# Kernel tuning notes

Measured on AMD Instinct MI355X. Metric: run time of the kernel, lower is better.

Reference implementation:

```python
import jax, jax.numpy as jnp
import numpy as np

GROUPS = 32
EPS = 1e-5

def group_norm(x, gamma, beta):
    B, C, H, W = x.shape
    xg = x.reshape(B, GROUPS, C // GROUPS, H, W)
    mean = xg.mean(axis=(2, 3, 4), keepdims=True)
    var = xg.var(axis=(2, 3, 4), keepdims=True)
    xn = ((xg - mean) * jax.lax.rsqrt(var + EPS)).reshape(B, C, H, W)
    return xn * gamma[None, :, None, None] + beta[None, :, None, None]

def conv1x1(x, w, b):
    # x: [B,C,H,W], w: [O,C], b: [O]
    return jnp.einsum('oc,bchw->bohw', w, x) + b[None, :, None, None]

def setup_inputs() -> dict:
    C = 256
    B, H, W = 32, 32, 32
    key = jax.random.key(0)
    ks = jax.random.split(key, 12)
    s = 0.02
    return {
        'x': jax.random.normal(ks[0], (B, C, H, W), jnp.float32),
        'gn_gamma': jnp.ones((C,), jnp.float32),
        'gn_beta': jnp.zeros((C,), jnp.float32),
        'w_qkv': jax.random.normal(ks[1], (3 * C, C), jnp.float32) * s,
        'b_qkv': jnp.zeros((3 * C,), jnp.float32),
        'w_proj': jax.random.normal(ks[2], (C, C), jnp.float32) * s,
        'b_proj': jnp.zeros((C,), jnp.float32),
        'w_se1': jax.random.normal(ks[3], (C // 4, C), jnp.float32) * s,
        'b_se1': jnp.zeros((C // 4,), jnp.float32),
        'w_se2': jax.random.normal(ks[4], (C, C // 4), jnp.float32) * s,
        'b_se2': jnp.zeros((C,), jnp.float32),
    }

def reference(x, gn_gamma, gn_beta, w_qkv, b_qkv, w_proj, b_proj, w_se1, b_se1, w_se2, b_se2):
    B, C, H, W = x.shape
    N = H * W
    residual = x
    xn = group_norm(x, gn_gamma, gn_beta)
    qkv = conv1x1(xn, w_qkv, b_qkv)            # [B,3C,H,W]
    q, k, v = jnp.split(qkv.reshape(B, 3 * C, N), 3, axis=1)  # each [B,C,N]
    scale = 1.0 / jnp.sqrt(jnp.float32(C))
    scores = jnp.einsum('bcn,bcm->bnm', q, k) * scale          # [B,N,N]
    attn = jax.nn.softmax(scores, axis=-1)
    # torch.bmm(v, attn^T): out[b,c,i] = sum_j v[b,c,j] * attn[b,i,j]
    x_attn = jnp.einsum('bcj,bij->bci', v, attn).reshape(B, C, H, W)
    x_attn = conv1x1(x_attn, w_proj, b_proj)
    # SE channel attention on the ORIGINAL x
    pooled = x.mean(axis=(2, 3))                               # [B,C]
    h1 = jax.nn.relu(pooled @ w_se1.T + b_se1)                 # [B,C//4]
    gate = jax.nn.sigmoid(h1 @ w_se2.T + b_se2)                # [B,C]
    return residual + x_attn * gate[:, :, None, None]
```

## Files before the change

### kernel.cpp

```cpp
#include <hip/hip_runtime.h>

typedef unsigned short u16;
typedef unsigned int u32;
typedef unsigned long long u64;
typedef __attribute__((ext_vector_type(4))) float vfloat4;
typedef __attribute__((ext_vector_type(8))) short vshort8;
typedef __attribute__((ext_vector_type(4))) short vshort4;

#define DEV __device__ __forceinline__

DEV u16 f2b(float f){
  u32 u = __builtin_bit_cast(u32, f);
  u = (u + 0x7fffu + ((u >> 16) & 1u)) >> 16;
  return (u16)u;
}

typedef __attribute__((address_space(3))) u32 as3u;
typedef __attribute__((address_space(1))) u32 as1u;
DEV void gll16(const u16* g, const u16* l){
  __builtin_amdgcn_global_load_lds((const as1u*)(u64)(uintptr_t)g,
                                   (as3u*)(u32)(u64)(uintptr_t)l, 16, 0, 0);
}

__global__ void k_stats(const float* __restrict__ x, float* __restrict__ osum, float* __restrict__ osq){
  int row = blockIdx.x;
  const vfloat4* xr = (const vfloat4*)(x + (size_t)row * 1024);
  vfloat4 v = xr[threadIdx.x];
  float s = v[0]+v[1]+v[2]+v[3];
  float q = v[0]*v[0]+v[1]*v[1]+v[2]*v[2]+v[3]*v[3];
  #pragma unroll
  for (int m = 1; m < 64; m <<= 1){ s += __shfl_xor(s, m); q += __shfl_xor(q, m); }
  __shared__ float ls[4], lq[4];
  int w = threadIdx.x >> 6;
  if ((threadIdx.x & 63) == 0){ ls[w] = s; lq[w] = q; }
  __syncthreads();
  if (threadIdx.x == 0){
    osum[row] = ls[0]+ls[1]+ls[2]+ls[3];
    osq[row]  = lq[0]+lq[1]+lq[2]+lq[3];
  }
}

__global__ void k_prep(const float* __restrict__ sum, const float* __restrict__ sq,
                       const float* __restrict__ gamma, const float* __restrict__ beta,
                       const float* __restrict__ w_se1, const float* __restrict__ b_se1,
                       const float* __restrict__ w_se2, const float* __restrict__ b_se2,
                       float* __restrict__ a_scale, float* __restrict__ bsh, float* __restrict__ gate){
  int b = blockIdx.x, c = threadIdx.x;
  __shared__ float ssh[256], qsh[256], pooled[256], h1[64], meang[32], rstdg[32];
  float s = sum[b*256 + c], q = sq[b*256 + c];
  ssh[c] = s; qsh[c] = q; pooled[c] = s * (1.f/1024.f);
  __syncthreads();
  if (c < 32){
    float gs = 0.f, gq = 0.f;
    #pragma unroll
    for (int i = 0; i < 8; i++){ gs += ssh[c*8+i]; gq += qsh[c*8+i]; }
    float mean = gs * (1.f/8192.f);
    float var  = gq * (1.f/8192.f) - mean*mean;
    meang[c] = mean; rstdg[c] = rsqrtf(var + 1e-5f);
  }
  __syncthreads();
  float rs = rstdg[c>>3], mn = meang[c>>3], g = gamma[c];
  a_scale[b*256+c] = rs*g;
  bsh[b*256+c]     = beta[c] - mn*rs*g;
  if (c < 64){
    float acc = b_se1[c];
    const float* wr = w_se1 + c*256;
    for (int i = 0; i < 256; i++) acc += pooled[i]*wr[i];
    h1[c] = fmaxf(acc, 0.f);
  }
  __syncthreads();
  float acc = b_se2[c];
  const float* wr2 = w_se2 + c*64;
  #pragma unroll
  for (int j = 0; j < 64; j++) acc += h1[j]*wr2[j];
  gate[b*256+c] = 1.f / (1.f + __expf(-acc));
}

__global__ void k_wcvt(const float* __restrict__ wq, const float* __restrict__ wp,
                       u16* __restrict__ wqb, u16* __restrict__ wpb){
  int i = blockIdx.x*256 + threadIdx.x;
  if (i < 196608) wqb[i] = f2b(wq[i]);
  else            wpb[i-196608] = f2b(wp[i-196608]);
}

__global__ void k_xt(const float* __restrict__ x, const float* __restrict__ a_s,
                     const float* __restrict__ bsh, u16* __restrict__ xs_t){
  __shared__ float t[64][65];
  int b = blockIdx.z, c0 = blockIdx.y*64, n0 = blockIdx.x*64;
  int tid = threadIdx.x;
  int rr = tid >> 4, cc = (tid & 15)*4;
  #pragma unroll
  for (int itr = 0; itr < 4; itr++){
    int r = rr + itr*16;
    int c = c0 + r;
    float a = a_s[b*256 + c], bs = bsh[b*256 + c];
    vfloat4 v = *(const vfloat4*)(x + ((size_t)(b*256 + c))*1024 + n0 + cc);
    t[r][cc]   = v[0]*a + bs;
    t[r][cc+1] = v[1]*a + bs;
    t[r][cc+2] = v[2]*a + bs;
    t[r][cc+3] = v[3]*a + bs;
  }
  __syncthreads();
  int cl = tid & 63, rg = tid >> 6;
  #pragma unroll
  for (int it2 = 0; it2 < 16; it2++){
    int nl = rg*16 + it2;
    xs_t[((size_t)b*1024 + n0 + nl)*256 + c0 + cl] = f2b(t[cl][nl]);
  }
}

__global__ __launch_bounds__(256) void k_qkv(
    const u16* __restrict__ wq_b, const u16* __restrict__ xs_t,
    const float* __restrict__ b_qkv,
    u16* __restrict__ qt, u16* __restrict__ kph, u16* __restrict__ vph){
  __shared__ u16 Alds[128*40];
  __shared__ u16 Blds[128*40];
  int b  = blockIdx.z;
  int o0 = blockIdx.y * 128;
  int n0 = blockIdx.x * 128;
  int tid = threadIdx.x;
  int w = tid >> 6, lane = tid & 63, lo = lane & 15, hi = lane >> 4;
  int wr = w >> 1, wc = w & 1;
  vfloat4 acc[4][4];
  #pragma unroll
  for (int i = 0; i < 4; i++)
    #pragma unroll
    for (int j = 0; j < 4; j++) acc[i][j] = vfloat4{0.f,0.f,0.f,0.f};

  for (int ks = 0; ks < 8; ks++){
    int c0 = ks*32;
    __syncthreads();
    #pragma unroll
    for (int i = 0; i < 2; i++){
      int cid = tid + i*256;
      int row = cid >> 2, h4 = cid & 3;
      vshort8 a = *(const vshort8*)(wq_b + (o0+row)*256 + c0 + h4*8);
      *(vshort8*)(Alds + row*40 + h4*8) = a;
      vshort8 bl = *(const vshort8*)(xs_t + ((size_t)b*1024 + n0 + row)*256 + c0 + h4*8);
      *(vshort8*)(Blds + row*40 + h4*8) = bl;
    }
    __syncthreads();
    vshort8 af[4], bf[4];
    #pragma unroll
    for (int of = 0; of < 4; of++) af[of] = *(const vshort8*)(Alds + (wr*64+of*16+lo)*40 + hi*8);
    #pragma unroll
    for (int nf = 0; nf < 4; nf++) bf[nf] = *(const vshort8*)(Blds + (wc*64+nf*16+lo)*40 + hi*8);
    #pragma unroll
    for (int of = 0; of < 4; of++)
      #pragma unroll
      for (int nf = 0; nf < 4; nf++)
        acc[of][nf] = __builtin_amdgcn_mfma_f32_16x16x32_bf16(af[of], bf[nf], acc[of][nf], 0, 0, 0);
  }

  int kind = blockIdx.y >> 1;
  #pragma unroll
  for (int of = 0; of < 4; of++){
    int ob = o0 + wr*64 + of*16 + hi*4;
    vfloat4 bq = *(const vfloat4*)(b_qkv + ob);
    #pragma unroll
    for (int nf = 0; nf < 4; nf++){
      int n = n0 + wc*64 + nf*16 + lo;
      int tile = n >> 5, j = n & 31;
      vfloat4 val = acc[of][nf];
      #pragma unroll
      for (int r = 0; r < 4; r++) val[r] += bq[r];
      if (kind == 0){
        vshort4 p;
        #pragma unroll
        for (int r = 0; r < 4; r++) p[r] = (short)f2b(val[r] * 0.09016844f);
        *(vshort4*)(qt + ((size_t)b*1024 + n)*256 + ob) = p;
      } else if (kind == 1){
        vshort4 p;
        #pragma unroll
        for (int r = 0; r < 4; r++) p[r] = (short)f2b(val[r]);
        int cx = (ob - 256) ^ ((j & 7) << 3);
        *(vshort4*)(kph + ((size_t)b << 18) + tile*8192 + j*256 + cx) = p;
      } else {
        int pos = ((j >> 2) & 3)*8 + ((j >> 4) << 2) + (j & 3);
        #pragma unroll
        for (int r = 0; r < 4; r++){
          int c = ob - 512 + r;
          int off = ((c >> 1) << 6) + (((((c & 1) << 5) + pos)) ^ (((c >> 1) & 7) << 3));
          vph[((size_t)b << 18) + tile*8192 + off] = f2b(val[r]);
        }
      }
    }
  }
}

__global__ __launch_bounds__(256, 1) void k_attn(
    const u16* __restrict__ qt, const u16* __restrict__ kph, const u16* __restrict__ vph,
    const u16* __restrict__ wp_b, const float* __restrict__ b_proj,
    const float* __restrict__ gate, const float* __restrict__ x,
    float* __restrict__ out){
  __shared__ u16 smem[33792];
  int b = blockIdx.y, i0 = blockIdx.x * 128;
  int tid = threadIdx.x, w = tid >> 6, lane = tid & 63, lo = lane & 15, hi = lane >> 4;

  vshort8 qf[2][8];
  #pragma unroll
  for (int f = 0; f < 2; f++){
    int iq = i0 + w*32 + f*16 + lo;
    #pragma unroll
    for (int ct = 0; ct < 8; ct++)
      qf[f][ct] = *(const vshort8*)(qt + ((size_t)b*1024 + iq)*256 + ct*32 + hi*8);
  }

  vfloat4 Oacc[16][2];
  #pragma unroll
  for (int i = 0; i < 16; i++){ Oacc[i][0] = vfloat4{0.f,0.f,0.f,0.f}; Oacc[i][1] = vfloat4{0.f,0.f,0.f,0.f}; }
  float m_run[2] = {-1e30f, -1e30f}, l_run[2] = {0.f, 0.f};

  int kswz = (lo & 7) << 3;
  int koff[8];
  #pragma unroll
  for (int ct = 0; ct < 8; ct++) koff[ct] = (ct*32 + hi*8) ^ kswz;
  int vbase = (lo >> 1)*64 + ((((lo & 1) << 5) + hi*8) ^ (((lo >> 1) & 7) << 3));

  const u16* kbat = kph + ((size_t)b << 18);
  const u16* vbat = vph + ((size_t)b << 18);

  auto STAGE = [&](int tt, int buf){
    const u16* ks = kbat + (size_t)tt * 8192;
    const u16* vs = vbat + (size_t)tt * 8192;
    u16* kd = smem + buf * 8192;
    u16* vd = smem + 16384 + buf * 8192;
    #pragma unroll
    for (int s = 0; s < 4; s++){
      int ch = (s*256 + tid) * 8;
      gll16(ks + ch, kd + ch);
      gll16(vs + ch, vd + ch);
    }
  };

  STAGE(0, 0);
  __syncthreads();

  for (int t = 0; t < 32; t++){
    int buf = t & 1;
    if (t < 31) STAGE(t + 1, buf ^ 1);
    const u16* Kb = smem + buf*8192;
    const u16* Vb = smem + 16384 + buf*8192;

    vfloat4 st[2][2];
    st[0][0] = vfloat4{0.f,0.f,0.f,0.f}; st[0][1] = vfloat4{0.f,0.f,0.f,0.f};
    st[1][0] = vfloat4{0.f,0.f,0.f,0.f}; st[1][1] = vfloat4{0.f,0.f,0.f,0.f};
    #pragma unroll
    for (int ct = 0; ct < 8; ct++){
      vshort8 k0 = *(const vshort8*)(Kb + lo*256 + koff[ct]);
      vshort8 k1 = *(const vshort8*)(Kb + (16 + lo)*256 + koff[ct]);
      st[0][0] = __builtin_amdgcn_mfma_f32_16x16x32_bf16(k0, qf[0][ct], st[0][0], 0,0,0);
      st[0][1] = __builtin_amdgcn_mfma_f32_16x16x32_bf16(k0, qf[1][ct], st[0][1], 0,0,0);
      st[1][0] = __builtin_amdgcn_mfma_f32_16x16x32_bf16(k1, qf[0][ct], st[1][0], 0,0,0);
      st[1][1] = __builtin_amdgcn_mfma_f32_16x16x32_bf16(k1, qf[1][ct], st[1][1], 0,0,0);
    }

    float pm[2];
    #pragma unroll
    for (int f = 0; f < 2; f++){
      float a = fmaxf(fmaxf(st[0][f][0], st[0][f][1]), fmaxf(st[0][f][2], st[0][f][3]));
      float c = fmaxf(fmaxf(st[1][f][0], st[1][f][1]), fmaxf(st[1][f][2], st[1][f][3]));
      float p = fmaxf(a, c);
      p = fmaxf(p, __shfl_xor(p, 16));
      p = fmaxf(p, __shfl_xor(p, 32));
      pm[f] = p;
    }
    bool ok = (pm[0] - m_run[0] <= 8.f) && (pm[1] - m_run[1] <= 8.f);
    if (!__all(ok)){
      #pragma unroll
      for (int f = 0; f < 2; f++){
        float mn = fmaxf(m_run[f], pm[f]);
        float corr = exp2f(m_run[f] - mn);
        #pragma unroll
        for (int i = 0; i < 16; i++) Oacc[i][f] *= corr;
        l_run[f] *= corr;
        m_run[f] = mn;
      }
    }
    vshort8 pf[2];
    #pragma unroll
    for (int f = 0; f < 2; f++){
      float p[8], ps = 0.f;
      #pragma unroll
      for (int e = 0; e < 4; e++){
        p[e]   = exp2f(st[0][f][e] - m_run[f]);
        p[4+e] = exp2f(st[1][f][e] - m_run[f]);
        ps += p[e] + p[4+e];
      }
      ps += __shfl_xor(ps, 16); ps += __shfl_xor(ps, 32);
      l_run[f] += ps;
      #pragma unroll
      for (int e2 = 0; e2 < 8; e2++) pf[f][e2] = (short)f2b(p[e2]);
    }

    #pragma unroll
    for (int ct2 = 0; ct2 < 16; ct2++){
      vshort8 vf = *(const vshort8*)(Vb + ct2*512 + vbase);
      Oacc[ct2][0] = __builtin_amdgcn_mfma_f32_16x16x32_bf16(vf, pf[0], Oacc[ct2][0], 0,0,0);
      Oacc[ct2][1] = __builtin_amdgcn_mfma_f32_16x16x32_bf16(vf, pf[1], Oacc[ct2][1], 0,0,0);
    }
    __syncthreads();
  }

  float inv[2] = {1.f / l_run[0], 1.f / l_run[1]};
  u16* Ol = smem;
  #pragma unroll
  for (int f = 0; f < 2; f++)
    #pragma unroll
    for (int ct2 = 0; ct2 < 16; ct2++){
      vshort4 p;
      #pragma unroll
      for (int r = 0; r < 4; r++) p[r] = (short)f2b(Oacc[ct2][f][r] * inv[f]);
      *(vshort4*)(Ol + (w*32 + f*16 + lo)*264 + ct2*16 + hi*4) = p;
    }
  __syncthreads();

  vfloat4 acc2[4][8];
  #pragma unroll
  for (int i = 0; i < 4; i++)
    #pragma unroll
    for (int j = 0; j < 8; j++) acc2[i][j] = vfloat4{0.f,0.f,0.f,0.f};
  #pragma unroll
  for (int ct = 0; ct < 8; ct++){
    vshort8 wf[4], ofr[8];
    #pragma unroll
    for (int o4 = 0; o4 < 4; o4++)
      wf[o4] = *(const vshort8*)(wp_b + (w*64 + o4*16 + lo)*256 + ct*32 + hi*8);
    #pragma unroll
    for (int i4 = 0; i4 < 8; i4++)
      ofr[i4] = *(const vshort8*)(Ol + (i4*16 + lo)*264 + ct*32 + hi*8);
    #pragma unroll
    for (int o4 = 0; o4 < 4; o4++)
      #pragma unroll
      for (int i4 = 0; i4 < 8; i4++)
        acc2[o4][i4] = __builtin_amdgcn_mfma_f32_16x16x32_bf16(wf[o4], ofr[i4], acc2[o4][i4], 0,0,0);
  }

  #pragma unroll
  for (int o4 = 0; o4 < 4; o4++){
    int ob = w*64 + o4*16 + hi*4;
    vfloat4 bp = *(const vfloat4*)(b_proj + ob);
    vfloat4 gt = *(const vfloat4*)(gate + b*256 + ob);
    #pragma unroll
    for (int i4 = 0; i4 < 8; i4++){
      int n = i0 + i4*16 + lo;
      #pragma unroll
      for (int r = 0; r < 4; r++){
        size_t idx = ((size_t)(b*256) + ob + r)*1024 + n;
        out[idx] = x[idx] + (acc2[o4][i4][r] + bp[r]) * gt[r];
      }
    }
  }
}

extern "C" void kernel_launch(void* const* d_in, const int* in_sizes, int n_in,
                              void* d_out, int out_size, void* d_ws, size_t ws_size,
                              hipStream_t stream){
  const float* x      = (const float*)d_in[0];
  const float* gamma  = (const float*)d_in[1];
  const float* beta   = (const float*)d_in[2];
  const float* w_qkv  = (const float*)d_in[3];
  const float* b_qkv  = (const float*)d_in[4];
  const float* w_proj = (const float*)d_in[5];
  const float* b_proj = (const float*)d_in[6];
  const float* w_se1  = (const float*)d_in[7];
  const float* b_se1  = (const float*)d_in[8];
  const float* w_se2  = (const float*)d_in[9];
  const float* b_se2  = (const float*)d_in[10];
  float* out = (float*)d_out;
  char* ws = (char*)d_ws;

  float* sum  = (float*)(ws + 0);
  float* sq   = (float*)(ws + 32768);
  float* a_s  = (float*)(ws + 65536);
  float* bsh  = (float*)(ws + 98304);
  float* gate = (float*)(ws + 131072);
  u16* wq_b   = (u16*)(ws + 163840);
  u16* wp_b   = (u16*)(ws + 557056);
  u16* xs_t   = (u16*)(ws + 688128);
  u16* qt     = (u16*)(ws + 17465344);
  u16* kph    = (u16*)(ws + 34242560);
  u16* vph    = (u16*)(ws + 51019776);

  k_stats<<<8192, 256, 0, stream>>>(x, sum, sq);
  k_wcvt <<<1024, 256, 0, stream>>>(w_qkv, w_proj, wq_b, wp_b);
  k_prep <<<32,   256, 0, stream>>>(sum, sq, gamma, beta, w_se1, b_se1, w_se2, b_se2, a_s, bsh, gate);
  k_xt   <<<dim3(16,4,32), 256, 0, stream>>>(x, a_s, bsh, xs_t);
  k_qkv  <<<dim3(8,6,32),  256, 0, stream>>>(wq_b, xs_t, b_qkv, qt, kph, vph);
  k_attn <<<dim3(8,32),    256, 0, stream>>>(qt, kph, vph, wp_b, b_proj, gate, x, out);
}
```

Before: 130.8 us.

## Split attention keys across wave pairs, load V directly from global, XCD-aware block mapping

The attention kernel now processes 64 query rows per block, with two wave groups each handling alternating key tiles (split-K). The partial softmax states and outputs are merged through shared memory at the end. V is stored in plain channel-major layout and read straight from global memory into registers instead of being staged in LDS, which halves the LDS footprint so two blocks can be resident per CU. Both the QKV and attention grids are flattened and remapped so each XCD handles whole batches for L2 locality, and s_setprio is added around the MFMA loops. The extra merge pass and the uncoalesced-style global V loads add cost and latency risk.

New measurement: 244.8 us. 1.87x slower.

```diff
diff --git a/kernel.cpp b/kernel.cpp
--- a/kernel.cpp
+++ b/kernel.cpp
@@ -112,12 +112,15 @@
 __global__ __launch_bounds__(256) void k_qkv(
     const u16* __restrict__ wq_b, const u16* __restrict__ xs_t,
     const float* __restrict__ b_qkv,
-    u16* __restrict__ qt, u16* __restrict__ kph, u16* __restrict__ vph){
+    u16* __restrict__ qt, u16* __restrict__ kph, u16* __restrict__ vv){
   __shared__ u16 Alds[128*40];
   __shared__ u16 Blds[128*40];
-  int b  = blockIdx.z;
-  int o0 = blockIdx.y * 128;
-  int n0 = blockIdx.x * 128;
+  int bid = blockIdx.x;
+  int xcd = bid & 7, idx = bid >> 3;
+  int b   = xcd*4 + idx/48;
+  int rem = idx % 48;
+  int o0 = (rem >> 3) * 128;
+  int n0 = (rem & 7) * 128;
   int tid = threadIdx.x;
   int w = tid >> 6, lane = tid & 63, lo = lane & 15, hi = lane >> 4;
   int wr = w >> 1, wc = w & 1;
@@ -152,7 +155,7 @@
         acc[of][nf] = __builtin_amdgcn_mfma_f32_16x16x32_bf16(af[of], bf[nf], acc[of][nf], 0, 0, 0);
   }
 
-  int kind = blockIdx.y >> 1;
+  int kind = o0 >> 8;
   #pragma unroll
   for (int of = 0; of < 4; of++){
     int ob = o0 + wr*64 + of*16 + hi*4;
@@ -176,31 +179,32 @@
         int cx = (ob - 256) ^ ((j & 7) << 3);
         *(vshort4*)(kph + ((size_t)b << 18) + tile*8192 + j*256 + cx) = p;
       } else {
-        int pos = ((j >> 2) & 3)*8 + ((j >> 4) << 2) + (j & 3);
         #pragma unroll
-        for (int r = 0; r < 4; r++){
-          int c = ob - 512 + r;
-          int off = ((c >> 1) << 6) + (((((c & 1) << 5) + pos)) ^ (((c >> 1) & 7) << 3));
-          vph[((size_t)b << 18) + tile*8192 + off] = f2b(val[r]);
-        }
+        for (int r = 0; r < 4; r++)
+          vv[((size_t)b*256 + (ob - 512 + r))*1024 + n] = f2b(val[r]);
       }
     }
   }
 }
 
-__global__ __launch_bounds__(256, 1) void k_attn(
-    const u16* __restrict__ qt, const u16* __restrict__ kph, const u16* __restrict__ vph,
+__global__ __launch_bounds__(256, 2) void k_attn(
+    const u16* __restrict__ qt, const u16* __restrict__ kph, const u16* __restrict__ vv,
     const u16* __restrict__ wp_b, const float* __restrict__ b_proj,
     const float* __restrict__ gate, const float* __restrict__ x,
     float* __restrict__ out){
-  __shared__ u16 smem[33792];
-  int b = blockIdx.y, i0 = blockIdx.x * 128;
+  __shared__ u16 smem[32768];
+  __shared__ float Ml[4][2][16], Ll[4][2][16];
+  int bid = blockIdx.x;
+  int xcd = bid & 7, idx = bid >> 3;
+  int b = xcd*4 + (idx >> 4);
+  int i0 = (idx & 15) * 64;
   int tid = threadIdx.x, w = tid >> 6, lane = tid & 63, lo = lane & 15, hi = lane >> 4;
+  int g = w >> 1, r = w & 1;
 
   vshort8 qf[2][8];
   #pragma unroll
   for (int f = 0; f < 2; f++){
-    int iq = i0 + w*32 + f*16 + lo;
+    int iq = i0 + r*32 + f*16 + lo;
     #pragma unroll
     for (int ct = 0; ct < 8; ct++)
       qf[f][ct] = *(const vshort8*)(qt + ((size_t)b*1024 + iq)*256 + ct*32 + hi*8);
@@ -215,36 +219,34 @@
   int koff[8];
   #pragma unroll
   for (int ct = 0; ct < 8; ct++) koff[ct] = (ct*32 + hi*8) ^ kswz;
-  int vbase = (lo >> 1)*64 + ((((lo & 1) << 5) + hi*8) ^ (((lo >> 1) & 7) << 3));
 
   const u16* kbat = kph + ((size_t)b << 18);
-  const u16* vbat = vph + ((size_t)b << 18);
-
-  auto STAGE = [&](int tt, int buf){
-    const u16* ks = kbat + (size_t)tt * 8192;
-    const u16* vs = vbat + (size_t)tt * 8192;
-    u16* kd = smem + buf * 8192;
-    u16* vd = smem + 16384 + buf * 8192;
-    #pragma unroll
-    for (int s = 0; s < 4; s++){
-      int ch = (s*256 + tid) * 8;
-      gll16(ks + ch, kd + ch);
-      gll16(vs + ch, vd + ch);
+  const u16* vvb  = vv  + ((size_t)b << 18);
+
+  auto STAGE = [&](int tile, int buf){
+    const u16* src = kbat + (size_t)tile * 8192;
+    u16* dst = smem + g*16384 + buf*8192;
+    int tg = tid & 127;
+    #pragma unroll
+    for (int s = 0; s < 8; s++){
+      int ch = (s*128 + tg)*8;
+      gll16(src + ch, dst + ch);
     }
   };
 
-  STAGE(0, 0);
-  __syncthreads();
-
-  for (int t = 0; t < 32; t++){
-    int buf = t & 1;
-    if (t < 31) STAGE(t + 1, buf ^ 1);
-    const u16* Kb = smem + buf*8192;
-    const u16* Vb = smem + 16384 + buf*8192;
+  STAGE(g, 0);
+  __syncthreads();
+
+  for (int rd = 0; rd < 16; rd++){
+    int buf = rd & 1;
+    int jt = (2*rd + g)*32;
+    if (rd < 15) STAGE(2*(rd+1) + g, buf ^ 1);
+    const u16* Kb = smem + g*16384 + buf*8192;
 
     vfloat4 st[2][2];
     st[0][0] = vfloat4{0.f,0.f,0.f,0.f}; st[0][1] = vfloat4{0.f,0.f,0.f,0.f};
     st[1][0] = vfloat4{0.f,0.f,0.f,0.f}; st[1][1] = vfloat4{0.f,0.f,0.f,0.f};
+    __builtin_amdgcn_s_setprio(1);
     #pragma unroll
     for (int ct = 0; ct < 8; ct++){
       vshort8 k0 = *(const vshort8*)(Kb + lo*256 + koff[ct]);
@@ -254,6 +256,15 @@
       st[1][0] = __builtin_amdgcn_mfma_f32_16x16x32_bf16(k1, qf[0][ct], st[1][0], 0,0,0);
       st[1][1] = __builtin_amdgcn_mfma_f32_16x16x32_bf16(k1, qf[1][ct], st[1][1], 0,0,0);
     }
+    __builtin_amdgcn_s_setprio(0);
+
+    vshort4 va0[8], va1[8];
+    #pragma unroll
+    for (int c8 = 0; c8 < 8; c8++){
+      const u16* vp = vvb + ((size_t)(c8*16 + lo))*1024 + jt + hi*4;
+      va0[c8] = *(const vshort4*)vp;
+      va1[c8] = *(const vshort4*)(vp + 16);
+    }
 
     float pm[2];
     #pragma unroll
@@ -265,8 +276,8 @@
       p = fmaxf(p, __shfl_xor(p, 32));
       pm[f] = p;
     }
-    bool ok = (pm[0] - m_run[0] <= 8.f) && (pm[1] - m_run[1] <= 8.f);
-    if (!__all(ok)){
+    bool okd = (pm[0] - m_run[0] <= 8.f) && (pm[1] - m_run[1] <= 8.f);
+    if (!__all(okd)){
       #pragma unroll
       for (int f = 0; f < 2; f++){
         float mn = fmaxf(m_run[f], pm[f]);
@@ -293,46 +304,95 @@
       for (int e2 = 0; e2 < 8; e2++) pf[f][e2] = (short)f2b(p[e2]);
     }
 
-    #pragma unroll
-    for (int ct2 = 0; ct2 < 16; ct2++){
-      vshort8 vf = *(const vshort8*)(Vb + ct2*512 + vbase);
-      Oacc[ct2][0] = __builtin_amdgcn_mfma_f32_16x16x32_bf16(vf, pf[0], Oacc[ct2][0], 0,0,0);
-      Oacc[ct2][1] = __builtin_amdgcn_mfma_f32_16x16x32_bf16(vf, pf[1], Oacc[ct2][1], 0,0,0);
-    }
+    __builtin_amdgcn_s_setprio(1);
+    #pragma unroll
+    for (int c8 = 0; c8 < 8; c8++){
+      const u16* vp = vvb + ((size_t)((c8+8)*16 + lo))*1024 + jt + hi*4;
+      vshort4 nb0 = *(const vshort4*)vp;
+      vshort4 nb1 = *(const vshort4*)(vp + 16);
+      vshort8 vf = __builtin_shufflevector(va0[c8], va1[c8], 0,1,2,3,4,5,6,7);
+      Oacc[c8][0] = __builtin_amdgcn_mfma_f32_16x16x32_bf16(vf, pf[0], Oacc[c8][0], 0,0,0);
+      Oacc[c8][1] = __builtin_amdgcn_mfma_f32_16x16x32_bf16(vf, pf[1], Oacc[c8][1], 0,0,0);
+      va0[c8] = nb0; va1[c8] = nb1;
+    }
+    #pragma unroll
+    for (int c8 = 0; c8 < 8; c8++){
+      vshort8 vf = __builtin_shufflevector(va0[c8], va1[c8], 0,1,2,3,4,5,6,7);
+      Oacc[c8+8][0] = __builtin_amdgcn_mfma_f32_16x16x32_bf16(vf, pf[0], Oacc[c8+8][0], 0,0,0);
+      Oacc[c8+8][1] = __builtin_amdgcn_mfma_f32_16x16x32_bf16(vf, pf[1], Oacc[c8+8][1], 0,0,0);
+    }
+    __builtin_amdgcn_s_setprio(0);
     __syncthreads();
   }
 
-  float inv[2] = {1.f / l_run[0], 1.f / l_run[1]};
+  if (hi == 0){ Ml[w][0][lo] = m_run[0]; Ml[w][1][lo] = m_run[1]; }
+  __syncthreads();
+  int pw = w ^ 2;
+  #pragma unroll
+  for (int f = 0; f < 2; f++){
+    float mp = Ml[pw][f][lo];
+    float mm = fmaxf(m_run[f], mp);
+    float sc = exp2f(m_run[f] - mm);
+    l_run[f] *= sc;
+    #pragma unroll
+    for (int i = 0; i < 16; i++) Oacc[i][f] *= sc;
+  }
+  if (hi == 0){ Ll[w][0][lo] = l_run[0]; Ll[w][1][lo] = l_run[1]; }
+  float* freg = (float*)smem;
+  if (g == 1){
+    #pragma unroll
+    for (int f = 0; f < 2; f++)
+      #pragma unroll
+      for (int i = 0; i < 16; i++)
+        *(vfloat4*)(freg + f*8192 + r*4096 + i*256 + lane*4) = Oacc[i][f];
+  }
+  __syncthreads();
+
   u16* Ol = smem;
-  #pragma unroll
-  for (int f = 0; f < 2; f++)
-    #pragma unroll
-    for (int ct2 = 0; ct2 < 16; ct2++){
-      vshort4 p;
-      #pragma unroll
-      for (int r = 0; r < 4; r++) p[r] = (short)f2b(Oacc[ct2][f][r] * inv[f]);
-      *(vshort4*)(Ol + (w*32 + f*16 + lo)*264 + ct2*16 + hi*4) = p;
-    }
-  __syncthreads();
-
-  vfloat4 acc2[4][8];
+  if (g == 0){
+    float inv[2];
+    #pragma unroll
+    for (int f = 0; f < 2; f++){
+      float lsum = l_run[f] + Ll[pw][f][lo];
+      inv[f] = 1.f / lsum;
+      #pragma unroll
+      for (int i = 0; i < 16; i++)
+        Oacc[i][f] += *(const vfloat4*)(freg + f*8192 + r*4096 + i*256 + lane*4);
+    }
+    #pragma unroll
+    for (int f = 0; f < 2; f++)
+      #pragma unroll
+      for (int i = 0; i < 16; i++){
+        vshort4 p;
+        #pragma unroll
+        for (int e = 0; e < 4; e++) p[e] = (short)f2b(Oacc[i][f][e] * inv[f]);
+        int irow = r*32 + f*16 + lo;
+        int coff = (i*16 + hi*4) ^ ((irow & 7) << 3);
+        *(vshort4*)(Ol + irow*256 + coff) = p;
+      }
+  }
+  __syncthreads();
+
+  vfloat4 acc2[4][4];
   #pragma unroll
   for (int i = 0; i < 4; i++)
     #pragma unroll
-    for (int j = 0; j < 8; j++) acc2[i][j] = vfloat4{0.f,0.f,0.f,0.f};
+    for (int j = 0; j < 4; j++) acc2[i][j] = vfloat4{0.f,0.f,0.f,0.f};
   #pragma unroll
   for (int ct = 0; ct < 8; ct++){
-    vshort8 wf[4], ofr[8];
+    vshort8 wf[4], ofr[4];
     #pragma unroll
     for (int o4 = 0; o4 < 4; o4++)
       wf[o4] = *(const vshort8*)(wp_b + (w*64 + o4*16 + lo)*256 + ct*32 + hi*8);
     #pragma unroll
-    for (int i4 = 0; i4 < 8; i4++)
-      ofr[i4] = *(const vshort8*)(Ol + (i4*16 + lo)*264 + ct*32 + hi*8);
+    for (int i4 = 0; i4 < 4; i4++){
+      int irow = i4*16 + lo;
+      ofr[i4] = *(const vshort8*)(Ol + irow*256 + ((ct*32 + hi*8) ^ ((irow & 7) << 3)));
+    }
     #pragma unroll
     for (int o4 = 0; o4 < 4; o4++)
       #pragma unroll
-      for (int i4 = 0; i4 < 8; i4++)
+      for (int i4 = 0; i4 < 4; i4++)
         acc2[o4][i4] = __builtin_amdgcn_mfma_f32_16x16x32_bf16(wf[o4], ofr[i4], acc2[o4][i4], 0,0,0);
   }
 
@@ -342,12 +402,12 @@
     vfloat4 bp = *(const vfloat4*)(b_proj + ob);
     vfloat4 gt = *(const vfloat4*)(gate + b*256 + ob);
     #pragma unroll
-    for (int i4 = 0; i4 < 8; i4++){
+    for (int i4 = 0; i4 < 4; i4++){
       int n = i0 + i4*16 + lo;
       #pragma unroll
-      for (int r = 0; r < 4; r++){
-        size_t idx = ((size_t)(b*256) + ob + r)*1024 + n;
-        out[idx] = x[idx] + (acc2[o4][i4][r] + bp[r]) * gt[r];
+      for (int e = 0; e < 4; e++){
+        size_t idxo = ((size_t)(b*256) + ob + e)*1024 + n;
+        out[idxo] = x[idxo] + (acc2[o4][i4][e] + bp[e]) * gt[e];
       }
     }
   }
@@ -380,12 +440,12 @@
   u16* xs_t   = (u16*)(ws + 688128);
   u16* qt     = (u16*)(ws + 17465344);
   u16* kph    = (u16*)(ws + 34242560);
-  u16* vph    = (u16*)(ws + 51019776);
+  u16* vv     = (u16*)(ws + 51019776);
 
   k_stats<<<8192, 256, 0, stream>>>(x, sum, sq);
   k_wcvt <<<1024, 256, 0, stream>>>(w_qkv, w_proj, wq_b, wp_b);
   k_prep <<<32,   256, 0, stream>>>(sum, sq, gamma, beta, w_se1, b_se1, w_se2, b_se2, a_s, bsh, gate);
   k_xt   <<<dim3(16,4,32), 256, 0, stream>>>(x, a_s, bsh, xs_t);
-  k_qkv  <<<dim3(8,6,32),  256, 0, stream>>>(wq_b, xs_t, b_qkv, qt, kph, vph);
-  k_attn <<<dim3(8,32),    256, 0, stream>>>(qt, kph, vph, wp_b, b_proj, gate, x, out);
-}
+  k_qkv  <<<1536, 256, 0, stream>>>(wq_b, xs_t, b_qkv, qt, kph, vv);
+  k_attn <<<512,  256, 0, stream>>>(qt, kph, vv, wp_b, b_proj, gate, x, out);
+}
```

## Triple-buffer K/V staging in attention and remap blocks to XCDs by batch

Applied to the files above, without the earlier changes.

The attention kernel moves from a double-buffered to a triple-buffered LDS pipeline. It issues the prefetch two tiles ahead after the QK MFMAs, and replaces the full __syncthreads with a partial vmcnt wait plus s_barrier. MFMA sections are wrapped in s_setprio. Both the QKV and attention kernels now use a flat 1D grid whose block indices map each batch onto a single XCD, aiming to improve L2 locality for shared K/V and weights. This raises LDS use to 96KB and depends on vmcnt counting being correct for the outstanding async loads.

Result: slower. 140.2 us (+7.2%).

```diff
diff --git a/kernel.cpp b/kernel.cpp
--- a/kernel.cpp
+++ b/kernel.cpp
@@ -115,9 +115,12 @@
     u16* __restrict__ qt, u16* __restrict__ kph, u16* __restrict__ vph){
   __shared__ u16 Alds[128*40];
   __shared__ u16 Blds[128*40];
-  int b  = blockIdx.z;
-  int o0 = blockIdx.y * 128;
-  int n0 = blockIdx.x * 128;
+  int bid = blockIdx.x;
+  int xcd = bid & 7, idx = bid >> 3;
+  int b   = xcd*4 + idx/48;
+  int rem = idx % 48;
+  int o0 = (rem >> 3) * 128;
+  int n0 = (rem & 7) * 128;
   int tid = threadIdx.x;
   int w = tid >> 6, lane = tid & 63, lo = lane & 15, hi = lane >> 4;
   int wr = w >> 1, wc = w & 1;
@@ -152,7 +155,7 @@
         acc[of][nf] = __builtin_amdgcn_mfma_f32_16x16x32_bf16(af[of], bf[nf], acc[of][nf], 0, 0, 0);
   }
 
-  int kind = blockIdx.y >> 1;
+  int kind = o0 >> 8;
   #pragma unroll
   for (int of = 0; of < 4; of++){
     int ob = o0 + wr*64 + of*16 + hi*4;
@@ -193,8 +196,11 @@
     const u16* __restrict__ wp_b, const float* __restrict__ b_proj,
     const float* __restrict__ gate, const float* __restrict__ x,
     float* __restrict__ out){
-  __shared__ u16 smem[33792];
-  int b = blockIdx.y, i0 = blockIdx.x * 128;
+  __shared__ u16 smem[49152];
+  int bid = blockIdx.x;
+  int xcd = bid & 7, idx = bid >> 3;
+  int b = xcd*4 + (idx >> 3);
+  int i0 = (idx & 7) * 128;
   int tid = threadIdx.x, w = tid >> 6, lane = tid & 63, lo = lane & 15, hi = lane >> 4;
 
   vshort8 qf[2][8];
@@ -220,11 +226,11 @@
   const u16* kbat = kph + ((size_t)b << 18);
   const u16* vbat = vph + ((size_t)b << 18);
 
-  auto STAGE = [&](int tt, int buf){
+  auto STAGE = [&](int tt, int slot){
     const u16* ks = kbat + (size_t)tt * 8192;
     const u16* vs = vbat + (size_t)tt * 8192;
-    u16* kd = smem + buf * 8192;
-    u16* vd = smem + 16384 + buf * 8192;
+    u16* kd = smem + slot * 8192;
+    u16* vd = smem + 24576 + slot * 8192;
     #pragma unroll
     for (int s = 0; s < 4; s++){
       int ch = (s*256 + tid) * 8;
@@ -234,17 +240,21 @@
   };
 
   STAGE(0, 0);
-  __syncthreads();
-
+  STAGE(1, 1);
+  asm volatile("s_waitcnt vmcnt(8)" ::: "memory");
+  __builtin_amdgcn_sched_barrier(0);
+  __builtin_amdgcn_s_barrier();
+  __builtin_amdgcn_sched_barrier(0);
+
+  int slot = 0;
   for (int t = 0; t < 32; t++){
-    int buf = t & 1;
-    if (t < 31) STAGE(t + 1, buf ^ 1);
-    const u16* Kb = smem + buf*8192;
-    const u16* Vb = smem + 16384 + buf*8192;
+    const u16* Kb = smem + slot*8192;
+    const u16* Vb = smem + 24576 + slot*8192;
 
     vfloat4 st[2][2];
     st[0][0] = vfloat4{0.f,0.f,0.f,0.f}; st[0][1] = vfloat4{0.f,0.f,0.f,0.f};
     st[1][0] = vfloat4{0.f,0.f,0.f,0.f}; st[1][1] = vfloat4{0.f,0.f,0.f,0.f};
+    __builtin_amdgcn_s_setprio(1);
     #pragma unroll
     for (int ct = 0; ct < 8; ct++){
       vshort8 k0 = *(const vshort8*)(Kb + lo*256 + koff[ct]);
@@ -254,6 +264,12 @@
       st[1][0] = __builtin_amdgcn_mfma_f32_16x16x32_bf16(k1, qf[0][ct], st[1][0], 0,0,0);
       st[1][1] = __builtin_amdgcn_mfma_f32_16x16x32_bf16(k1, qf[1][ct], st[1][1], 0,0,0);
     }
+    __builtin_amdgcn_s_setprio(0);
+
+    if (t < 30){
+      int s2 = slot + 2; if (s2 >= 3) s2 -= 3;
+      STAGE(t + 2, s2);
+    }
 
     float pm[2];
     #pragma unroll
@@ -265,8 +281,8 @@
       p = fmaxf(p, __shfl_xor(p, 32));
       pm[f] = p;
     }
-    bool ok = (pm[0] - m_run[0] <= 8.f) && (pm[1] - m_run[1] <= 8.f);
-    if (!__all(ok)){
+    bool okd = (pm[0] - m_run[0] <= 8.f) && (pm[1] - m_run[1] <= 8.f);
+    if (!__all(okd)){
       #pragma unroll
       for (int f = 0; f < 2; f++){
         float mn = fmaxf(m_run[f], pm[f]);
@@ -293,16 +309,30 @@
       for (int e2 = 0; e2 < 8; e2++) pf[f][e2] = (short)f2b(p[e2]);
     }
 
+    __builtin_amdgcn_s_setprio(1);
     #pragma unroll
     for (int ct2 = 0; ct2 < 16; ct2++){
       vshort8 vf = *(const vshort8*)(Vb + ct2*512 + vbase);
       Oacc[ct2][0] = __builtin_amdgcn_mfma_f32_16x16x32_bf16(vf, pf[0], Oacc[ct2][0], 0,0,0);
       Oacc[ct2][1] = __builtin_amdgcn_mfma_f32_16x16x32_bf16(vf, pf[1], Oacc[ct2][1], 0,0,0);
     }
-    __syncthreads();
+    __builtin_amdgcn_s_setprio(0);
+
+    if (t < 30){
+      asm volatile("s_waitcnt vmcnt(8)" ::: "memory");
+    } else {
+      asm volatile("s_waitcnt vmcnt(0)" ::: "memory");
+    }
+    __builtin_amdgcn_sched_barrier(0);
+    __builtin_amdgcn_s_barrier();
+    __builtin_amdgcn_sched_barrier(0);
+
+    slot++; if (slot == 3) slot = 0;
   }
 
   float inv[2] = {1.f / l_run[0], 1.f / l_run[1]};
+  asm volatile("s_waitcnt vmcnt(0)" ::: "memory");
+  __syncthreads();
   u16* Ol = smem;
   #pragma unroll
   for (int f = 0; f < 2; f++)
@@ -345,9 +375,9 @@
     for (int i4 = 0; i4 < 8; i4++){
       int n = i0 + i4*16 + lo;
       #pragma unroll
-      for (int r = 0; r < 4; r++){
-        size_t idx = ((size_t)(b*256) + ob + r)*1024 + n;
-        out[idx] = x[idx] + (acc2[o4][i4][r] + bp[r]) * gt[r];
+      for (int e = 0; e < 4; e++){
+        size_t idxo = ((size_t)(b*256) + ob + e)*1024 + n;
+        out[idxo] = x[idxo] + (acc2[o4][i4][e] + bp[e]) * gt[e];
       }
     }
   }
@@ -386,6 +416,6 @@
   k_wcvt <<<1024, 256, 0, stream>>>(w_qkv, w_proj, wq_b, wp_b);
   k_prep <<<32,   256, 0, stream>>>(sum, sq, gamma, beta, w_se1, b_se1, w_se2, b_se2, a_s, bsh, gate);
   k_xt   <<<dim3(16,4,32), 256, 0, stream>>>(x, a_s, bsh, xs_t);
-  k_qkv  <<<dim3(8,6,32),  256, 0, stream>>>(wq_b, xs_t, b_qkv, qt, kph, vph);
-  k_attn <<<dim3(8,32),    256, 0, stream>>>(qt, kph, vph, wp_b, b_proj, gate, x, out);
-}
+  k_qkv  <<<1536, 256, 0, stream>>>(wq_b, xs_t, b_qkv, qt, kph, vph);
+  k_attn <<<256,  256, 0, stream>>>(qt, kph, vph, wp_b, b_proj, gate, x, out);
+}
```

## Switch attention to 32x32x16 MFMA with new K/V swizzles and XCD-aware block mapping

Applied to the files above, without the earlier changes.

Rewrites the flash-attention inner loop to use 32x32x16 bf16 MFMA tiles instead of 16x16x32, with one query row per lane pair. The K and V layouts written by the QKV kernel are re-swizzled to match the new fragment access pattern. Both the QKV and attention grids become 1D with an XCD-aware remap so that blocks of the same batch share an XCD's L2. It also adds s_setprio around the MFMA sections and packs P with v_cvt_pk_bf16_f32. The aim is fewer MFMA and LDS instructions and less shuffle reduction per tile, at the cost of larger accumulator register pressure and the risk of subtle layout mismatches.

New measurement: 120.0 us (median of 3 runs). 1.09x faster.

```diff
diff --git a/kernel.cpp b/kernel.cpp
--- a/kernel.cpp
+++ b/kernel.cpp
@@ -4,8 +4,10 @@
 typedef unsigned int u32;
 typedef unsigned long long u64;
 typedef __attribute__((ext_vector_type(4))) float vfloat4;
+typedef __attribute__((ext_vector_type(16))) float vfloat16;
 typedef __attribute__((ext_vector_type(8))) short vshort8;
 typedef __attribute__((ext_vector_type(4))) short vshort4;
+typedef __attribute__((ext_vector_type(4))) u32 vuint4;
 
 #define DEV __device__ __forceinline__
 
@@ -115,9 +117,12 @@
     u16* __restrict__ qt, u16* __restrict__ kph, u16* __restrict__ vph){
   __shared__ u16 Alds[128*40];
   __shared__ u16 Blds[128*40];
-  int b  = blockIdx.z;
-  int o0 = blockIdx.y * 128;
-  int n0 = blockIdx.x * 128;
+  int bid = blockIdx.x;
+  int xcd = bid & 7, idx = bid >> 3;
+  int b   = xcd*4 + idx/48;
+  int rem = idx % 48;
+  int o0 = (rem >> 3) * 128;
+  int n0 = (rem & 7) * 128;
   int tid = threadIdx.x;
   int w = tid >> 6, lane = tid & 63, lo = lane & 15, hi = lane >> 4;
   int wr = w >> 1, wc = w & 1;
@@ -152,7 +157,7 @@
         acc[of][nf] = __builtin_amdgcn_mfma_f32_16x16x32_bf16(af[of], bf[nf], acc[of][nf], 0, 0, 0);
   }
 
-  int kind = blockIdx.y >> 1;
+  int kind = o0 >> 8;
   #pragma unroll
   for (int of = 0; of < 4; of++){
     int ob = o0 + wr*64 + of*16 + hi*4;
@@ -173,14 +178,17 @@
         vshort4 p;
         #pragma unroll
         for (int r = 0; r < 4; r++) p[r] = (short)f2b(val[r]);
-        int cx = (ob - 256) ^ ((j & 7) << 3);
-        *(vshort4*)(kph + ((size_t)b << 18) + tile*8192 + j*256 + cx) = p;
+        int cx = ob - 256;
+        int slot = (cx >> 3) ^ j;
+        *(vshort4*)(kph + ((size_t)b << 18) + tile*8192 + j*256 + slot*8 + (cx & 7)) = p;
       } else {
-        int pos = ((j >> 2) & 3)*8 + ((j >> 4) << 2) + (j & 3);
+        int m2 = (j >> 4) & 1, q2 = (j >> 2) & 1;
+        int e2 = (j & 3) | ((j & 8) >> 1);
         #pragma unroll
         for (int r = 0; r < 4; r++){
           int c = ob - 512 + r;
-          int off = ((c >> 1) << 6) + (((((c & 1) << 5) + pos)) ^ (((c >> 1) & 7) << 3));
+          int a2 = c >> 2;
+          int off = a2*128 + (c & 3)*32 + ((((m2 << 1) | q2) ^ (a2 & 3)) << 3) + e2;
           vph[((size_t)b << 18) + tile*8192 + off] = f2b(val[r]);
         }
       }
@@ -194,28 +202,34 @@
     const float* __restrict__ gate, const float* __restrict__ x,
     float* __restrict__ out){
   __shared__ u16 smem[33792];
-  int b = blockIdx.y, i0 = blockIdx.x * 128;
+  int bid = blockIdx.x;
+  int xcd = bid & 7, idx = bid >> 3;
+  int b = xcd*4 + (idx >> 3);
+  int i0 = (idx & 7) * 128;
   int tid = threadIdx.x, w = tid >> 6, lane = tid & 63, lo = lane & 15, hi = lane >> 4;
-
-  vshort8 qf[2][8];
-  #pragma unroll
-  for (int f = 0; f < 2; f++){
-    int iq = i0 + w*32 + f*16 + lo;
-    #pragma unroll
-    for (int ct = 0; ct < 8; ct++)
-      qf[f][ct] = *(const vshort8*)(qt + ((size_t)b*1024 + iq)*256 + ct*32 + hi*8);
-  }
-
-  vfloat4 Oacc[16][2];
-  #pragma unroll
-  for (int i = 0; i < 16; i++){ Oacc[i][0] = vfloat4{0.f,0.f,0.f,0.f}; Oacc[i][1] = vfloat4{0.f,0.f,0.f,0.f}; }
-  float m_run[2] = {-1e30f, -1e30f}, l_run[2] = {0.f, 0.f};
-
-  int kswz = (lo & 7) << 3;
-  int koff[8];
-  #pragma unroll
-  for (int ct = 0; ct < 8; ct++) koff[ct] = (ct*32 + hi*8) ^ kswz;
-  int vbase = (lo >> 1)*64 + ((((lo & 1) << 5) + hi*8) ^ (((lo >> 1) & 7) << 3));
+  int jj = lane & 31, q = lane >> 5;
+
+  int iq = i0 + w*32 + jj;
+  vshort8 qf[16];
+  #pragma unroll
+  for (int kk = 0; kk < 16; kk++)
+    qf[kk] = *(const vshort8*)(qt + ((size_t)b*1024 + iq)*256 + kk*16 + q*8);
+
+  vfloat16 Oacc[8];
+  #pragma unroll
+  for (int ct = 0; ct < 8; ct++)
+    #pragma unroll
+    for (int e = 0; e < 16; e++) Oacc[ct][e] = 0.f;
+  float m_run = -1e30f, l_run = 0.f;
+
+  int koff[16];
+  #pragma unroll
+  for (int kk = 0; kk < 16; kk++)
+    koff[kk] = jj*256 + ((((kk << 1) | q) ^ jj) << 3);
+  int a0 = jj >> 2;
+  int vb = a0*128 + (jj & 3)*32;
+  int xm0 = ((q)       ^ (a0 & 3)) << 3;
+  int xm1 = ((2 | q)   ^ (a0 & 3)) << 3;
 
   const u16* kbat = kph + ((size_t)b << 18);
   const u16* vbat = vph + ((size_t)b << 18);
@@ -242,76 +256,73 @@
     const u16* Kb = smem + buf*8192;
     const u16* Vb = smem + 16384 + buf*8192;
 
-    vfloat4 st[2][2];
-    st[0][0] = vfloat4{0.f,0.f,0.f,0.f}; st[0][1] = vfloat4{0.f,0.f,0.f,0.f};
-    st[1][0] = vfloat4{0.f,0.f,0.f,0.f}; st[1][1] = vfloat4{0.f,0.f,0.f,0.f};
+    vfloat16 stA, stB;
+    #pragma unroll
+    for (int e = 0; e < 16; e++){ stA[e] = 0.f; stB[e] = 0.f; }
+    __builtin_amdgcn_s_setprio(1);
+    #pragma unroll
+    for (int kk = 0; kk < 16; kk += 2){
+      vshort8 k0 = *(const vshort8*)(Kb + koff[kk]);
+      vshort8 k1 = *(const vshort8*)(Kb + koff[kk+1]);
+      stA = __builtin_amdgcn_mfma_f32_32x32x16_bf16(k0, qf[kk],   stA, 0,0,0);
+      stB = __builtin_amdgcn_mfma_f32_32x32x16_bf16(k1, qf[kk+1], stB, 0,0,0);
+    }
+    __builtin_amdgcn_s_setprio(0);
+    vfloat16 st = stA + stB;
+
+    float pml = st[0];
+    #pragma unroll
+    for (int e = 1; e < 16; e++) pml = fmaxf(pml, st[e]);
+    if (!__all(pml - m_run <= 8.f)){
+      float po = fmaxf(pml, __shfl_xor(pml, 32));
+      float mn = fmaxf(m_run, po);
+      float corr = exp2f(m_run - mn);
+      #pragma unroll
+      for (int ct = 0; ct < 8; ct++) Oacc[ct] *= corr;
+      l_run *= corr;
+      m_run = mn;
+    }
+
+    float pv[16]; float ls = 0.f;
+    #pragma unroll
+    for (int e = 0; e < 16; e++){ pv[e] = exp2f(st[e] - m_run); ls += pv[e]; }
+    l_run += ls;
+
+    u32 pw[8];
+    #pragma unroll
+    for (int rr = 0; rr < 4; rr++){
+      asm("v_cvt_pk_bf16_f32 %0, %1, %2" : "=v"(pw[rr])   : "v"(pv[2*rr]),   "v"(pv[2*rr+1]));
+      asm("v_cvt_pk_bf16_f32 %0, %1, %2" : "=v"(pw[4+rr]) : "v"(pv[8+2*rr]), "v"(pv[8+2*rr+1]));
+    }
+    vshort8 pf0 = __builtin_bit_cast(vshort8, vuint4{pw[0], pw[1], pw[2], pw[3]});
+    vshort8 pf1 = __builtin_bit_cast(vshort8, vuint4{pw[4], pw[5], pw[6], pw[7]});
+
+    __builtin_amdgcn_s_setprio(1);
     #pragma unroll
     for (int ct = 0; ct < 8; ct++){
-      vshort8 k0 = *(const vshort8*)(Kb + lo*256 + koff[ct]);
-      vshort8 k1 = *(const vshort8*)(Kb + (16 + lo)*256 + koff[ct]);
-      st[0][0] = __builtin_amdgcn_mfma_f32_16x16x32_bf16(k0, qf[0][ct], st[0][0], 0,0,0);
-      st[0][1] = __builtin_amdgcn_mfma_f32_16x16x32_bf16(k0, qf[1][ct], st[0][1], 0,0,0);
-      st[1][0] = __builtin_amdgcn_mfma_f32_16x16x32_bf16(k1, qf[0][ct], st[1][0], 0,0,0);
-      st[1][1] = __builtin_amdgcn_mfma_f32_16x16x32_bf16(k1, qf[1][ct], st[1][1], 0,0,0);
-    }
-
-    float pm[2];
-    #pragma unroll
-    for (int f = 0; f < 2; f++){
-      float a = fmaxf(fmaxf(st[0][f][0], st[0][f][1]), fmaxf(st[0][f][2], st[0][f][3]));
-      float c = fmaxf(fmaxf(st[1][f][0], st[1][f][1]), fmaxf(st[1][f][2], st[1][f][3]));
-      float p = fmaxf(a, c);
-      p = fmaxf(p, __shfl_xor(p, 16));
-      p = fmaxf(p, __shfl_xor(p, 32));
-      pm[f] = p;
-    }
-    bool ok = (pm[0] - m_run[0] <= 8.f) && (pm[1] - m_run[1] <= 8.f);
-    if (!__all(ok)){
-      #pragma unroll
-      for (int f = 0; f < 2; f++){
-        float mn = fmaxf(m_run[f], pm[f]);
-        float corr = exp2f(m_run[f] - mn);
-        #pragma unroll
-        for (int i = 0; i < 16; i++) Oacc[i][f] *= corr;
-        l_run[f] *= corr;
-        m_run[f] = mn;
-      }
-    }
-    vshort8 pf[2];
-    #pragma unroll
-    for (int f = 0; f < 2; f++){
-      float p[8], ps = 0.f;
-      #pragma unroll
-      for (int e = 0; e < 4; e++){
-        p[e]   = exp2f(st[0][f][e] - m_run[f]);
-        p[4+e] = exp2f(st[1][f][e] - m_run[f]);
-        ps += p[e] + p[4+e];
-      }
-      ps += __shfl_xor(ps, 16); ps += __shfl_xor(ps, 32);
-      l_run[f] += ps;
-      #pragma unroll
-      for (int e2 = 0; e2 < 8; e2++) pf[f][e2] = (short)f2b(p[e2]);
-    }
-
-    #pragma unroll
-    for (int ct2 = 0; ct2 < 16; ct2++){
-      vshort8 vf = *(const vshort8*)(Vb + ct2*512 + vbase);
-      Oacc[ct2][0] = __builtin_amdgcn_mfma_f32_16x16x32_bf16(vf, pf[0], Oacc[ct2][0], 0,0,0);
-      Oacc[ct2][1] = __builtin_amdgcn_mfma_f32_16x16x32_bf16(vf, pf[1], Oacc[ct2][1], 0,0,0);
-    }
+      vshort8 v0 = *(const vshort8*)(Vb + ct*1024 + vb + xm0);
+      vshort8 v1 = *(const vshort8*)(Vb + ct*1024 + vb + xm1);
+      Oacc[ct] = __builtin_amdgcn_mfma_f32_32x32x16_bf16(v0, pf0, Oacc[ct], 0,0,0);
+      Oacc[ct] = __builtin_amdgcn_mfma_f32_32x32x16_bf16(v1, pf1, Oacc[ct], 0,0,0);
+    }
+    __builtin_amdgcn_s_setprio(0);
     __syncthreads();
   }
 
-  float inv[2] = {1.f / l_run[0], 1.f / l_run[1]};
+  float lt = l_run + __shfl_xor(l_run, 32);
+  float inv = 1.f / lt;
+
+  __syncthreads();
   u16* Ol = smem;
   #pragma unroll
-  for (int f = 0; f < 2; f++)
-    #pragma unroll
-    for (int ct2 = 0; ct2 < 16; ct2++){
-      vshort4 p;
-      #pragma unroll
-      for (int r = 0; r < 4; r++) p[r] = (short)f2b(Oacc[ct2][f][r] * inv[f]);
-      *(vshort4*)(Ol + (w*32 + f*16 + lo)*264 + ct2*16 + hi*4) = p;
+  for (int ct = 0; ct < 8; ct++)
+    #pragma unroll
+    for (int qd = 0; qd < 4; qd++){
+      vshort4 pk;
+      #pragma unroll
+      for (int e3 = 0; e3 < 4; e3++) pk[e3] = (short)f2b(Oacc[ct][4*qd + e3] * inv);
+      int cb = ct*32 + 8*qd + 4*q;
+      *(vshort4*)(Ol + (w*32 + jj)*264 + cb) = pk;
     }
   __syncthreads();
 
@@ -345,9 +356,9 @@
     for (int i4 = 0; i4 < 8; i4++){
       int n = i0 + i4*16 + lo;
       #pragma unroll
-      for (int r = 0; r < 4; r++){
-        size_t idx = ((size_t)(b*256) + ob + r)*1024 + n;
-        out[idx] = x[idx] + (acc2[o4][i4][r] + bp[r]) * gt[r];
+      for (int e = 0; e < 4; e++){
+        size_t idxo = ((size_t)(b*256) + ob + e)*1024 + n;
+        out[idxo] = x[idxo] + (acc2[o4][i4][e] + bp[e]) * gt[e];
       }
     }
   }
@@ -386,6 +397,6 @@
   k_wcvt <<<1024, 256, 0, stream>>>(w_qkv, w_proj, wq_b, wp_b);
   k_prep <<<32,   256, 0, stream>>>(sum, sq, gamma, beta, w_se1, b_se1, w_se2, b_se2, a_s, bsh, gate);
   k_xt   <<<dim3(16,4,32), 256, 0, stream>>>(x, a_s, bsh, xs_t);
-  k_qkv  <<<dim3(8,6,32),  256, 0, stream>>>(wq_b, xs_t, b_qkv, qt, kph, vph);
-  k_attn <<<dim3(8,32),    256, 0, stream>>>(qt, kph, vph, wp_b, b_proj, gate, x, out);
-}
+  k_qkv  <<<1536, 256, 0, stream>>>(wq_b, xs_t, b_qkv, qt, kph, vph);
+  k_attn <<<256,  256, 0, stream>>>(qt, kph, vph, wp_b, b_proj, gate, x, out);
+}
```
